# Kernel optimization log

Hardware: AMD Instinct MI355X
Metric: run time of the kernel (lower is better)

Reference implementation:

```python
import jax, jax.numpy as jnp
import numpy as np

B, C, H, W = 128, 1, 256, 256
IN_DIM = 256      # = W
HID = 1024
OUT_DIM = 10


def _linear_init(key, fan_in, shape):
    bound = 1.0 / np.sqrt(fan_in)
    return jax.random.uniform(key, shape, jnp.float32, -bound, bound)


def _make_layer_params(key, in_dim, hid):
    # 4 gates in fixed order: forget, input, cell, output
    ks = jax.random.split(key, 4)
    Wi = _linear_init(ks[0], in_dim, (in_dim, 4 * hid))
    Wh = _linear_init(ks[1], hid, (hid, 4 * hid))
    bi = _linear_init(ks[2], in_dim, (4 * hid,))
    bh = _linear_init(ks[3], hid, (4 * hid,))
    return Wi, Wh, bi, bh


def setup_inputs() -> dict:
    key = jax.random.key(0)
    kx, k1, k2, kc, kh1, kc1, kh2, kc2 = jax.random.split(key, 8)
    Wi1, Wh1, bi1, bh1 = _make_layer_params(k1, IN_DIM, HID)
    Wi2, Wh2, bi2, bh2 = _make_layer_params(k2, HID, HID)
    kcw, kcb = jax.random.split(kc)
    Wc = _linear_init(kcw, HID, (HID, OUT_DIM))
    bc = _linear_init(kcb, HID, (OUT_DIM,))
    return {
        "x": jax.random.normal(kx, (B, C, H, W), jnp.float32),
        "h01": jax.random.normal(kh1, (B, HID), jnp.float32),
        "c01": jax.random.normal(kc1, (B, HID), jnp.float32),
        "h02": jax.random.normal(kh2, (B, HID), jnp.float32),
        "c02": jax.random.normal(kc2, (B, HID), jnp.float32),
        "Wi1": Wi1, "Wh1": Wh1, "bi1": bi1, "bh1": bh1,
        "Wi2": Wi2, "Wh2": Wh2, "bi2": bi2, "bh2": bh2,
        "Wc": Wc, "bc": bc,
    }


def _lstm_layer(x, Wi, Wh, bi, bh, h0, c0):
    """x: [B,T,D] -> hidden outputs [B,T,H]. Gate order: f, i, g(cell), o."""
    hid = Wh.shape[0]
    # Batched input projection for all timesteps at once: [B,T,4H]
    xproj = jnp.einsum('btd,dg->btg', x, Wi) + bi

    def step(carry, xp_t):
        h, c = carry
        z = xp_t + h @ Wh + bh                       # [B,4H]
        f, i, g, o = jnp.split(z, 4, axis=-1)
        f = jax.nn.sigmoid(f)
        i = jax.nn.sigmoid(i)
        g = jnp.tanh(g)
        o = jax.nn.sigmoid(o)
        c_new = c * f + i * g
        h_new = jnp.tanh(c_new) * o
        return (h_new, c_new), h_new

    _, hs = jax.lax.scan(step, (h0, c0), jnp.swapaxes(xproj, 0, 1))  # hs: [T,B,H]
    return jnp.swapaxes(hs, 0, 1)


def reference(x, h01, c01, h02, c02,
              Wi1, Wh1, bi1, bh1,
              Wi2, Wh2, bi2, bh2,
              Wc, bc):
    b = x.shape[0]
    seq = x.shape[1] * x.shape[2]                    # C*H
    xs = x.reshape(b, seq, IN_DIM)                   # [B,T,D]
    out1 = _lstm_layer(xs, Wi1, Wh1, bi1, bh1, h01, c01)
    out2 = _lstm_layer(out1, Wi2, Wh2, bi2, bh2, h02, c02)
    y = out2[:, -1, :] @ Wc + bc                     # [B, OUT_DIM]
    return y
```

## Files before the change

kernel.cpp:

```cpp
#include <hip/hip_runtime.h>

typedef _Float16 f16;
typedef __attribute__((ext_vector_type(8))) _Float16 f16x8;
typedef __attribute__((ext_vector_type(4))) _Float16 f16x4;
typedef __attribute__((ext_vector_type(16))) float f32x16;

#define B_ 128
#define HID_ 1024
#define BH_ (B_ * HID_)

__global__ __launch_bounds__(256) void k_cast_x(const float* __restrict__ x,
                                                f16* __restrict__ xf) {
    size_t g = (size_t)blockIdx.x * blockDim.x + threadIdx.x;
    size_t e = g * 4;
    const int d = (int)(e & 255);
    const int t = (int)((e >> 8) & 255);
    const int b = (int)(e >> 16);
    float4 v = ((const float4*)x)[g];
    f16x4 o = {(f16)v.x, (f16)v.y, (f16)v.z, (f16)v.w};
    *(f16x4*)(xf + ((size_t)t * B_ + b) * 256 + d) = o;
}

__global__ __launch_bounds__(256) void k_pack(const float* __restrict__ src,
                                              f16* __restrict__ dst,
                                              int Ktot, int koff) {
    __shared__ float tile[64][65];
    const int tx = threadIdx.x & 63, ty = threadIdx.x >> 6;
    const int r0 = blockIdx.y * 64, c0 = blockIdx.x * 64;
    #pragma unroll
    for (int r = ty; r < 64; r += 4)
        tile[r][tx] = src[(size_t)(r0 + r) * 4096 + c0 + tx];
    __syncthreads();
    const int k = koff + r0 + tx;
    #pragma unroll
    for (int rr = ty; rr < 64; rr += 4) {
        const int col = c0 + rr;
        const int g = col >> 10, hg = col & 1023;
        const int wg = hg >> 3, pcl = (g << 3) | (hg & 7);
        size_t off = ((size_t)wg * 32 + pcl) * Ktot + (((k >> 3) ^ (pcl & 7)) << 3) + (k & 7);
        dst[off] = (f16)tile[tx][rr];
    }
}

__global__ __launch_bounds__(256) void k_prep(
    const float* __restrict__ bi1, const float* __restrict__ bh1,
    const float* __restrict__ bi2, const float* __restrict__ bh2,
    const float* __restrict__ h01, const float* __restrict__ h02,
    float* b1, float* b2, f16* h1r, f16* h2b, unsigned int* cnt) {
    int i = blockIdx.x * blockDim.x + threadIdx.x;
    if (i == 0) *cnt = 0u;
    if (i < 4096) { b1[i] = bi1[i] + bh1[i]; b2[i] = bi2[i] + bh2[i]; }
    if (i < BH_) {
        h1r[i] = (f16)h01[i];
        h2b[BH_ + i] = (f16)h02[i];
    }
}

__device__ __forceinline__ void publish8(f16* p, f16x4 v) {
    union { f16x4 h; unsigned long long u; } cv;
    cv.h = v;
    __hip_atomic_store((unsigned long long*)p, cv.u,
                       __ATOMIC_RELAXED, __HIP_MEMORY_SCOPE_AGENT);
}

__global__ __launch_bounds__(256, 1) void k_persist(
    const f16* __restrict__ Wp1,
    const f16* __restrict__ Wp2,
    const f16* __restrict__ xall,
    f16* h1r, f16* h2b,
    float* h2f,
    const float* __restrict__ b1, const float* __restrict__ b2,
    const float* __restrict__ c01, const float* __restrict__ c02,
    unsigned int* cnt) {
    __shared__ __align__(16) unsigned char smem[163840];
    f16*   Wl = (f16*)smem;
    float* zl = (float*)(smem + 131072);

    const int bid = blockIdx.x;
    const int layer = bid >> 7;
    const int wg = bid & 127;
    const int tid = threadIdx.x;
    const int lane = tid & 63, wave = tid >> 6, hl = lane >> 5;
    const int K = layer ? 2048 : 1280;

    {
        const f16* Wsrc = layer ? (Wp2 + (size_t)wg * 32 * 2048)
                                : (Wp1 + (size_t)wg * 32 * 1280);
        const int n = 32 * K / 8;
        for (int i = tid; i < n; i += 256)
            ((f16x8*)Wl)[i] = ((const f16x8*)Wsrc)[i];
    }

    const int m = tid & 127, half = tid >> 7;
    const int ug0 = wg * 8 + half * 4;
    const float* csrc = layer ? c02 : c01;
    float4 creg = *(const float4*)(csrc + (size_t)m * HID_ + ug0);
    float biasr[4][4];
    {
        const float* bsrc = layer ? b2 : b1;
        #pragma unroll
        for (int g = 0; g < 4; ++g)
            #pragma unroll
            for (int j = 0; j < 4; ++j)
                biasr[g][j] = bsrc[g * HID_ + ug0 + j];
    }
    __syncthreads();

    const int pcl = lane & 31;
    const int swz = pcl & 7;
    f16* hmine = (layer ? h2b : h1r);

    f32x16 acc[4];
    #pragma unroll
    for (int mt = 0; mt < 4; ++mt)
        #pragma unroll
        for (int r = 0; r < 16; ++r) acc[mt][r] = 0.f;

    if (layer == 0) {
        const f16* A0n = xall;
        for (int c = wave; c < 16; c += 4) {
            const int ic = c * 2 + hl;
            f16x8 bfrag = *(const f16x8*)(Wl + pcl * 1280 + ((ic ^ swz) << 3));
            const f16* ap = A0n + (size_t)pcl * 256 + c * 16 + hl * 8;
            #pragma unroll
            for (int mt = 0; mt < 4; ++mt) {
                f16x8 afrag = *(const f16x8*)(ap + (size_t)mt * 32 * 256);
                acc[mt] = __builtin_amdgcn_mfma_f32_32x32x16_f16(afrag, bfrag, acc[mt], 0, 0, 0);
            }
        }
    }

    for (int s = 0; s <= 256; ++s) {
        const bool active = layer == 0 ? (s < 256) : (s >= 1);
        if (active) {
            if (layer == 0) {
                const f16* A1 = h1r + (size_t)(s & 1) * BH_;
                for (int c = 16 + wave; c < 80; c += 4) {
                    const int ic = c * 2 + hl;
                    f16x8 bfrag = *(const f16x8*)(Wl + pcl * 1280 + ((ic ^ swz) << 3));
                    const f16* ap = A1 + (size_t)pcl * HID_ + (c * 16 - 256) + hl * 8;
                    #pragma unroll
                    for (int mt = 0; mt < 4; ++mt) {
                        f16x8 afrag = *(const f16x8*)(ap + (size_t)mt * 32 * HID_);
                        acc[mt] = __builtin_amdgcn_mfma_f32_32x32x16_f16(afrag, bfrag, acc[mt], 0, 0, 0);
                    }
                }
            } else {
                const f16* A0 = h1r + (size_t)(s & 1) * BH_;
                const f16* A1 = h2b + (size_t)(s & 1) * BH_;
                for (int c = wave; c < 128; c += 4) {
                    const f16* Ab = (c < 64) ? A0 : A1;
                    const int kloc = (c & 63) * 16;
                    const int ic = c * 2 + hl;
                    f16x8 bfrag = *(const f16x8*)(Wl + pcl * 2048 + ((ic ^ swz) << 3));
                    const f16* ap = Ab + (size_t)pcl * HID_ + kloc + hl * 8;
                    #pragma unroll
                    for (int mt = 0; mt < 4; ++mt) {
                        f16x8 afrag = *(const f16x8*)(ap + (size_t)mt * 32 * HID_);
                        acc[mt] = __builtin_amdgcn_mfma_f32_32x32x16_f16(afrag, bfrag, acc[mt], 0, 0, 0);
                    }
                }
            }

            float* Z = zl + (size_t)(wave & 1) * 4096;
            if (wave < 2) {
                #pragma unroll
                for (int mt = 0; mt < 4; ++mt)
                    #pragma unroll
                    for (int r = 0; r < 16; ++r) {
                        const int row = mt * 32 + (r & 3) + 8 * (r >> 2) + 4 * hl;
                        Z[row * 32 + (pcl ^ (row & 31))] = acc[mt][r];
                    }
            }
            __syncthreads();
            if (wave >= 2) {
                #pragma unroll
                for (int mt = 0; mt < 4; ++mt)
                    #pragma unroll
                    for (int r = 0; r < 16; ++r) {
                        const int row = mt * 32 + (r & 3) + 8 * (r >> 2) + 4 * hl;
                        Z[row * 32 + (pcl ^ (row & 31))] += acc[mt][r];
                    }
            }
            __syncthreads();

            float zg4[4][4];
            #pragma unroll
            for (int g = 0; g < 4; ++g)
                #pragma unroll
                for (int j = 0; j < 4; ++j) {
                    const int cc = g * 8 + half * 4 + j;
                    const int idx = m * 32 + (cc ^ (m & 31));
                    zg4[g][j] = zl[idx] + zl[4096 + idx] + biasr[g][j];
                }
            f16x4 hout;
            float4 hf;
            #pragma unroll
            for (int j = 0; j < 4; ++j) {
                const float fg = 1.f / (1.f + __expf(-zg4[0][j]));
                const float ig = 1.f / (1.f + __expf(-zg4[1][j]));
                const float gg = 1.f - 2.f / (__expf(2.f * zg4[2][j]) + 1.f);
                const float og = 1.f / (1.f + __expf(-zg4[3][j]));
                float cv = j == 0 ? creg.x : j == 1 ? creg.y : j == 2 ? creg.z : creg.w;
                const float cn = cv * fg + ig * gg;
                if (j == 0) creg.x = cn; else if (j == 1) creg.y = cn;
                else if (j == 2) creg.z = cn; else creg.w = cn;
                const float h = (1.f - 2.f / (__expf(2.f * cn) + 1.f)) * og;
                hout[j] = (f16)h;
                ((float*)&hf)[j] = h;
            }
            publish8(hmine + (size_t)((s + 1) & 1) * BH_ + (size_t)m * HID_ + ug0, hout);
            if (layer == 1 && s == 256)
                *(float4*)(h2f + (size_t)m * HID_ + ug0) = hf;
        }

        if (s < 256) {
            asm volatile("s_waitcnt vmcnt(0)" ::: "memory");
            __syncthreads();
            if (tid == 0)
                __hip_atomic_fetch_add(cnt, 1u, __ATOMIC_RELAXED, __HIP_MEMORY_SCOPE_AGENT);

            #pragma unroll
            for (int mt = 0; mt < 4; ++mt)
                #pragma unroll
                for (int r = 0; r < 16; ++r) acc[mt][r] = 0.f;
            if (layer == 0 && s + 1 < 256) {
                const f16* A0n = xall + (size_t)(s + 1) * (B_ * 256);
                for (int c = wave; c < 16; c += 4) {
                    const int ic = c * 2 + hl;
                    f16x8 bfrag = *(const f16x8*)(Wl + pcl * 1280 + ((ic ^ swz) << 3));
                    const f16* ap = A0n + (size_t)pcl * 256 + c * 16 + hl * 8;
                    #pragma unroll
                    for (int mt = 0; mt < 4; ++mt) {
                        f16x8 afrag = *(const f16x8*)(ap + (size_t)mt * 32 * 256);
                        acc[mt] = __builtin_amdgcn_mfma_f32_32x32x16_f16(afrag, bfrag, acc[mt], 0, 0, 0);
                    }
                }
            }

            if (tid == 0) {
                const unsigned int target = 256u * (unsigned)(s + 1);
                while (__hip_atomic_load(cnt, __ATOMIC_RELAXED, __HIP_MEMORY_SCOPE_AGENT) < target)
                    __builtin_amdgcn_s_sleep(8);
                __builtin_amdgcn_fence(__ATOMIC_ACQUIRE, "agent");
            }
            __syncthreads();
        }
    }
}

__global__ __launch_bounds__(64) void k_final(const float* __restrict__ h2f,
                                              const float* __restrict__ Wc,
                                              const float* __restrict__ bc,
                                              float* __restrict__ y) {
    const int b = blockIdx.x, lane = threadIdx.x;
    float acc[10] = {0, 0, 0, 0, 0, 0, 0, 0, 0, 0};
    for (int k = lane; k < HID_; k += 64) {
        const float h = h2f[b * HID_ + k];
        #pragma unroll
        for (int j = 0; j < 10; ++j) acc[j] = fmaf(h, Wc[k * 10 + j], acc[j]);
    }
    #pragma unroll
    for (int off = 32; off; off >>= 1)
        #pragma unroll
        for (int j = 0; j < 10; ++j) acc[j] += __shfl_down(acc[j], off);
    if (lane == 0) {
        #pragma unroll
        for (int j = 0; j < 10; ++j) y[b * 10 + j] = acc[j] + bc[j];
    }
}

extern "C" void kernel_launch(void* const* d_in, const int* in_sizes, int n_in,
                              void* d_out, int out_size, void* d_ws, size_t ws_size,
                              hipStream_t stream) {
    (void)in_sizes; (void)n_in; (void)out_size; (void)ws_size;
    const float* x   = (const float*)d_in[0];
    const float* h01 = (const float*)d_in[1];
    const float* c01 = (const float*)d_in[2];
    const float* h02 = (const float*)d_in[3];
    const float* c02 = (const float*)d_in[4];
    const float* Wi1 = (const float*)d_in[5];
    const float* Wh1 = (const float*)d_in[6];
    const float* bi1 = (const float*)d_in[7];
    const float* bh1 = (const float*)d_in[8];
    const float* Wi2 = (const float*)d_in[9];
    const float* Wh2 = (const float*)d_in[10];
    const float* bi2 = (const float*)d_in[11];
    const float* bh2 = (const float*)d_in[12];
    const float* Wc  = (const float*)d_in[13];
    const float* bc  = (const float*)d_in[14];
    float* y = (float*)d_out;

    char* w = (char*)d_ws;
    f16*   xall = (f16*)(w + 0);
    f16*   Wp1  = (f16*)(w + 16777216);
    f16*   Wp2  = (f16*)(w + 27262976);
    f16*   h1r  = (f16*)(w + 44040192);
    f16*   h2b  = (f16*)(w + 44564480);
    float* h2f  = (float*)(w + 45088768);
    float* b1   = (float*)(w + 45613056);
    float* b2   = (float*)(w + 45629440);
    unsigned int* cnt = (unsigned int*)(w + 45645824);

    k_cast_x<<<8192, 256, 0, stream>>>(x, xall);
    k_pack<<<dim3(64, 4),  256, 0, stream>>>(Wi1, Wp1, 1280, 0);
    k_pack<<<dim3(64, 16), 256, 0, stream>>>(Wh1, Wp1, 1280, 256);
    k_pack<<<dim3(64, 16), 256, 0, stream>>>(Wi2, Wp2, 2048, 0);
    k_pack<<<dim3(64, 16), 256, 0, stream>>>(Wh2, Wp2, 2048, 1024);
    k_prep<<<512, 256, 0, stream>>>(bi1, bh1, bi2, bh2, h01, h02, b1, b2, h1r, h2b, cnt);

    k_persist<<<256, 256, 0, stream>>>(Wp1, Wp2, xall, h1r, h2b, h2f, b1, b2, c01, c02, cnt);

    k_final<<<128, 64, 0, stream>>>(h2f, Wc, bc, y);
}
```

Before: 7.917 ms.

## Replace global step barrier with per-block flag dataflow sync and 512-thread blocks

Replaces the single global atomic counter barrier with per-workgroup progress flags per layer, polled by one wave across all 128 flags. Layer 0 can now run up to three steps ahead of layer 1 using a 4-slot h1 ring, and layer 1 starts its h1 half of the GEMM before waiting on its own layer's h2. Blocks grow from 256 to 512 threads (8 waves split the K loop), and the partial-sum reduction uses LDS atomics. This is meant to remove lockstep barrier stalls and skew between layers, at the cost of more polling traffic and LDS atomic contention.

```diff
diff --git a/kernel.cpp b/kernel.cpp
--- a/kernel.cpp
+++ b/kernel.cpp
@@ -46,32 +46,42 @@
     const float* __restrict__ bi1, const float* __restrict__ bh1,
     const float* __restrict__ bi2, const float* __restrict__ bh2,
     const float* __restrict__ h01, const float* __restrict__ h02,
-    float* b1, float* b2, f16* h1r, f16* h2b, unsigned int* cnt) {
+    float* b1, float* b2, f16* h1r, f16* h2b,
+    unsigned* flags1, unsigned* flags2) {
     int i = blockIdx.x * blockDim.x + threadIdx.x;
-    if (i == 0) *cnt = 0u;
+    if (i < 128) { flags1[i] = 0u; flags2[i] = 0u; }
     if (i < 4096) { b1[i] = bi1[i] + bh1[i]; b2[i] = bi2[i] + bh2[i]; }
     if (i < BH_) {
         h1r[i] = (f16)h01[i];
-        h2b[BH_ + i] = (f16)h02[i];
-    }
-}
-
-__device__ __forceinline__ void publish8(f16* p, f16x4 v) {
-    union { f16x4 h; unsigned long long u; } cv;
-    cv.h = v;
-    __hip_atomic_store((unsigned long long*)p, cv.u,
+        h2b[i] = (f16)h02[i];
+    }
+}
+
+__device__ __forceinline__ void publish4(f16* p, f16 a, f16 b) {
+    union { struct { f16 x, y; } h; unsigned u; } cv;
+    cv.h.x = a; cv.h.y = b;
+    __hip_atomic_store((unsigned*)p, cv.u,
                        __ATOMIC_RELAXED, __HIP_MEMORY_SCOPE_AGENT);
 }
 
-__global__ __launch_bounds__(256, 1) void k_persist(
-    const f16* __restrict__ Wp1,
-    const f16* __restrict__ Wp2,
+__device__ __forceinline__ void poll_ge(const unsigned* flags, int target) {
+    if (target <= 0) return;
+    const int l2 = (threadIdx.x & 63) << 1;
+    for (;;) {
+        int f0 = (int)__hip_atomic_load(flags + l2,     __ATOMIC_RELAXED, __HIP_MEMORY_SCOPE_AGENT);
+        int f1 = (int)__hip_atomic_load(flags + l2 + 1, __ATOMIC_RELAXED, __HIP_MEMORY_SCOPE_AGENT);
+        if (__all(f0 >= target && f1 >= target)) break;
+        __builtin_amdgcn_s_sleep(2);
+    }
+}
+
+__global__ __launch_bounds__(512, 1) void k_persist(
+    const f16* __restrict__ Wp1, const f16* __restrict__ Wp2,
     const f16* __restrict__ xall,
-    f16* h1r, f16* h2b,
-    float* h2f,
+    f16* h1r, f16* h2b, float* h2f,
     const float* __restrict__ b1, const float* __restrict__ b2,
     const float* __restrict__ c01, const float* __restrict__ c02,
-    unsigned int* cnt) {
+    unsigned* flags1, unsigned* flags2) {
     __shared__ __align__(16) unsigned char smem[163840];
     f16*   Wl = (f16*)smem;
     float* zl = (float*)(smem + 131072);
@@ -81,34 +91,34 @@
     const int wg = bid & 127;
     const int tid = threadIdx.x;
     const int lane = tid & 63, wave = tid >> 6, hl = lane >> 5;
+    const int pcl = lane & 31, swz = pcl & 7;
     const int K = layer ? 2048 : 1280;
 
     {
         const f16* Wsrc = layer ? (Wp2 + (size_t)wg * 32 * 2048)
                                 : (Wp1 + (size_t)wg * 32 * 1280);
         const int n = 32 * K / 8;
-        for (int i = tid; i < n; i += 256)
+        for (int i = tid; i < n; i += 512)
             ((f16x8*)Wl)[i] = ((const f16x8*)Wsrc)[i];
     }
 
-    const int m = tid & 127, half = tid >> 7;
-    const int ug0 = wg * 8 + half * 4;
+    const int m = tid & 127, q = tid >> 7;
+    const int u0 = q * 2;
+    const int ug0 = wg * 8 + u0;
     const float* csrc = layer ? c02 : c01;
-    float4 creg = *(const float4*)(csrc + (size_t)m * HID_ + ug0);
-    float biasr[4][4];
+    float c0 = csrc[(size_t)m * HID_ + ug0];
+    float c1v = csrc[(size_t)m * HID_ + ug0 + 1];
+    float biasr[4][2];
     {
         const float* bsrc = layer ? b2 : b1;
         #pragma unroll
-        for (int g = 0; g < 4; ++g)
-            #pragma unroll
-            for (int j = 0; j < 4; ++j)
-                biasr[g][j] = bsrc[g * HID_ + ug0 + j];
-    }
-    __syncthreads();
-
-    const int pcl = lane & 31;
-    const int swz = pcl & 7;
-    f16* hmine = (layer ? h2b : h1r);
+        for (int g = 0; g < 4; ++g) {
+            biasr[g][0] = bsrc[g * HID_ + ug0];
+            biasr[g][1] = bsrc[g * HID_ + ug0 + 1];
+        }
+    }
+    unsigned* myflags = layer ? flags2 : flags1;
+    f16* hmine = layer ? h2b : h1r;
 
     f32x16 acc[4];
     #pragma unroll
@@ -116,136 +126,136 @@
         #pragma unroll
         for (int r = 0; r < 16; ++r) acc[mt][r] = 0.f;
 
-    if (layer == 0) {
-        const f16* A0n = xall;
-        for (int c = wave; c < 16; c += 4) {
-            const int ic = c * 2 + hl;
-            f16x8 bfrag = *(const f16x8*)(Wl + pcl * 1280 + ((ic ^ swz) << 3));
-            const f16* ap = A0n + (size_t)pcl * 256 + c * 16 + hl * 8;
-            #pragma unroll
-            for (int mt = 0; mt < 4; ++mt) {
-                f16x8 afrag = *(const f16x8*)(ap + (size_t)mt * 32 * 256);
-                acc[mt] = __builtin_amdgcn_mfma_f32_32x32x16_f16(afrag, bfrag, acc[mt], 0, 0, 0);
-            }
-        }
-    }
-
-    for (int s = 0; s <= 256; ++s) {
-        const bool active = layer == 0 ? (s < 256) : (s >= 1);
-        if (active) {
-            if (layer == 0) {
-                const f16* A1 = h1r + (size_t)(s & 1) * BH_;
-                for (int c = 16 + wave; c < 80; c += 4) {
-                    const int ic = c * 2 + hl;
-                    f16x8 bfrag = *(const f16x8*)(Wl + pcl * 1280 + ((ic ^ swz) << 3));
-                    const f16* ap = A1 + (size_t)pcl * HID_ + (c * 16 - 256) + hl * 8;
-                    #pragma unroll
-                    for (int mt = 0; mt < 4; ++mt) {
-                        f16x8 afrag = *(const f16x8*)(ap + (size_t)mt * 32 * HID_);
-                        acc[mt] = __builtin_amdgcn_mfma_f32_32x32x16_f16(afrag, bfrag, acc[mt], 0, 0, 0);
-                    }
-                }
-            } else {
-                const f16* A0 = h1r + (size_t)(s & 1) * BH_;
-                const f16* A1 = h2b + (size_t)(s & 1) * BH_;
-                for (int c = wave; c < 128; c += 4) {
-                    const f16* Ab = (c < 64) ? A0 : A1;
-                    const int kloc = (c & 63) * 16;
-                    const int ic = c * 2 + hl;
-                    f16x8 bfrag = *(const f16x8*)(Wl + pcl * 2048 + ((ic ^ swz) << 3));
-                    const f16* ap = Ab + (size_t)pcl * HID_ + kloc + hl * 8;
-                    #pragma unroll
-                    for (int mt = 0; mt < 4; ++mt) {
-                        f16x8 afrag = *(const f16x8*)(ap + (size_t)mt * 32 * HID_);
-                        acc[mt] = __builtin_amdgcn_mfma_f32_32x32x16_f16(afrag, bfrag, acc[mt], 0, 0, 0);
-                    }
-                }
-            }
-
-            float* Z = zl + (size_t)(wave & 1) * 4096;
-            if (wave < 2) {
-                #pragma unroll
-                for (int mt = 0; mt < 4; ++mt)
-                    #pragma unroll
-                    for (int r = 0; r < 16; ++r) {
-                        const int row = mt * 32 + (r & 3) + 8 * (r >> 2) + 4 * hl;
-                        Z[row * 32 + (pcl ^ (row & 31))] = acc[mt][r];
-                    }
+    __syncthreads();
+
+    for (int t = 0; t < 256; ++t) {
+        if (layer == 0) {
+            const f16* A0 = xall + (size_t)t * (B_ * 256);
+            for (int c = wave; c < 16; c += 8) {
+                const int ic = c * 2 + hl;
+                f16x8 bfrag = *(const f16x8*)(Wl + pcl * 1280 + ((ic ^ swz) << 3));
+                const f16* ap = A0 + (size_t)pcl * 256 + c * 16 + hl * 8;
+                #pragma unroll
+                for (int mt = 0; mt < 4; ++mt) {
+                    f16x8 afrag = *(const f16x8*)(ap + (size_t)mt * 32 * 256);
+                    acc[mt] = __builtin_amdgcn_mfma_f32_32x32x16_f16(afrag, bfrag, acc[mt], 0, 0, 0);
+                }
+            }
+            if (wave == 0) {
+                poll_ge(flags1, t);
+                __builtin_amdgcn_fence(__ATOMIC_ACQUIRE, "agent");
+            } else if (wave == 1) {
+                poll_ge(flags2, t - 3);
             }
             __syncthreads();
-            if (wave >= 2) {
-                #pragma unroll
-                for (int mt = 0; mt < 4; ++mt)
-                    #pragma unroll
-                    for (int r = 0; r < 16; ++r) {
-                        const int row = mt * 32 + (r & 3) + 8 * (r >> 2) + 4 * hl;
-                        Z[row * 32 + (pcl ^ (row & 31))] += acc[mt][r];
-                    }
+            const f16* A1 = h1r + (size_t)(t & 3) * BH_;
+            for (int c = 16 + wave; c < 80; c += 8) {
+                const int ic = c * 2 + hl;
+                f16x8 bfrag = *(const f16x8*)(Wl + pcl * 1280 + ((ic ^ swz) << 3));
+                const f16* ap = A1 + (size_t)pcl * HID_ + (c * 16 - 256) + hl * 8;
+                #pragma unroll
+                for (int mt = 0; mt < 4; ++mt) {
+                    f16x8 afrag = *(const f16x8*)(ap + (size_t)mt * 32 * HID_);
+                    acc[mt] = __builtin_amdgcn_mfma_f32_32x32x16_f16(afrag, bfrag, acc[mt], 0, 0, 0);
+                }
+            }
+        } else {
+            if (wave == 0) {
+                poll_ge(flags1, t + 1);
+                __builtin_amdgcn_fence(__ATOMIC_ACQUIRE, "agent");
             }
             __syncthreads();
-
-            float zg4[4][4];
-            #pragma unroll
-            for (int g = 0; g < 4; ++g)
-                #pragma unroll
-                for (int j = 0; j < 4; ++j) {
-                    const int cc = g * 8 + half * 4 + j;
-                    const int idx = m * 32 + (cc ^ (m & 31));
-                    zg4[g][j] = zl[idx] + zl[4096 + idx] + biasr[g][j];
-                }
-            f16x4 hout;
-            float4 hf;
-            #pragma unroll
-            for (int j = 0; j < 4; ++j) {
-                const float fg = 1.f / (1.f + __expf(-zg4[0][j]));
-                const float ig = 1.f / (1.f + __expf(-zg4[1][j]));
-                const float gg = 1.f - 2.f / (__expf(2.f * zg4[2][j]) + 1.f);
-                const float og = 1.f / (1.f + __expf(-zg4[3][j]));
-                float cv = j == 0 ? creg.x : j == 1 ? creg.y : j == 2 ? creg.z : creg.w;
-                const float cn = cv * fg + ig * gg;
-                if (j == 0) creg.x = cn; else if (j == 1) creg.y = cn;
-                else if (j == 2) creg.z = cn; else creg.w = cn;
-                const float h = (1.f - 2.f / (__expf(2.f * cn) + 1.f)) * og;
-                hout[j] = (f16)h;
-                ((float*)&hf)[j] = h;
-            }
-            publish8(hmine + (size_t)((s + 1) & 1) * BH_ + (size_t)m * HID_ + ug0, hout);
-            if (layer == 1 && s == 256)
-                *(float4*)(h2f + (size_t)m * HID_ + ug0) = hf;
-        }
-
-        if (s < 256) {
-            asm volatile("s_waitcnt vmcnt(0)" ::: "memory");
+            const f16* A0 = h1r + (size_t)((t + 1) & 3) * BH_;
+            for (int c = wave; c < 64; c += 8) {
+                const int ic = c * 2 + hl;
+                f16x8 bfrag = *(const f16x8*)(Wl + pcl * 2048 + ((ic ^ swz) << 3));
+                const f16* ap = A0 + (size_t)pcl * HID_ + c * 16 + hl * 8;
+                #pragma unroll
+                for (int mt = 0; mt < 4; ++mt) {
+                    f16x8 afrag = *(const f16x8*)(ap + (size_t)mt * 32 * HID_);
+                    acc[mt] = __builtin_amdgcn_mfma_f32_32x32x16_f16(afrag, bfrag, acc[mt], 0, 0, 0);
+                }
+            }
+            if (wave == 0) {
+                poll_ge(flags2, t);
+                __builtin_amdgcn_fence(__ATOMIC_ACQUIRE, "agent");
+            }
             __syncthreads();
-            if (tid == 0)
-                __hip_atomic_fetch_add(cnt, 1u, __ATOMIC_RELAXED, __HIP_MEMORY_SCOPE_AGENT);
-
+            const f16* A1 = h2b + (size_t)(t & 1) * BH_;
+            for (int c = 64 + wave; c < 128; c += 8) {
+                const int ic = c * 2 + hl;
+                f16x8 bfrag = *(const f16x8*)(Wl + pcl * 2048 + ((ic ^ swz) << 3));
+                const f16* ap = A1 + (size_t)pcl * HID_ + (c * 16 - 1024) + hl * 8;
+                #pragma unroll
+                for (int mt = 0; mt < 4; ++mt) {
+                    f16x8 afrag = *(const f16x8*)(ap + (size_t)mt * 32 * HID_);
+                    acc[mt] = __builtin_amdgcn_mfma_f32_32x32x16_f16(afrag, bfrag, acc[mt], 0, 0, 0);
+                }
+            }
+        }
+
+        float* Z = zl + (size_t)(wave & 1) * 4096;
+        if (wave < 2) {
             #pragma unroll
             for (int mt = 0; mt < 4; ++mt)
                 #pragma unroll
-                for (int r = 0; r < 16; ++r) acc[mt][r] = 0.f;
-            if (layer == 0 && s + 1 < 256) {
-                const f16* A0n = xall + (size_t)(s + 1) * (B_ * 256);
-                for (int c = wave; c < 16; c += 4) {
-                    const int ic = c * 2 + hl;
-                    f16x8 bfrag = *(const f16x8*)(Wl + pcl * 1280 + ((ic ^ swz) << 3));
-                    const f16* ap = A0n + (size_t)pcl * 256 + c * 16 + hl * 8;
-                    #pragma unroll
-                    for (int mt = 0; mt < 4; ++mt) {
-                        f16x8 afrag = *(const f16x8*)(ap + (size_t)mt * 32 * 256);
-                        acc[mt] = __builtin_amdgcn_mfma_f32_32x32x16_f16(afrag, bfrag, acc[mt], 0, 0, 0);
-                    }
-                }
-            }
-
-            if (tid == 0) {
-                const unsigned int target = 256u * (unsigned)(s + 1);
-                while (__hip_atomic_load(cnt, __ATOMIC_RELAXED, __HIP_MEMORY_SCOPE_AGENT) < target)
-                    __builtin_amdgcn_s_sleep(8);
-                __builtin_amdgcn_fence(__ATOMIC_ACQUIRE, "agent");
-            }
-            __syncthreads();
-        }
+                for (int r = 0; r < 16; ++r) {
+                    const int row = mt * 32 + (r & 3) + 8 * (r >> 2) + 4 * hl;
+                    Z[row * 32 + (pcl ^ (row & 31))] = acc[mt][r];
+                }
+        }
+        __syncthreads();
+        if (wave >= 2) {
+            #pragma unroll
+            for (int mt = 0; mt < 4; ++mt)
+                #pragma unroll
+                for (int r = 0; r < 16; ++r) {
+                    const int row = mt * 32 + (r & 3) + 8 * (r >> 2) + 4 * hl;
+                    atomicAdd(&Z[row * 32 + (pcl ^ (row & 31))], acc[mt][r]);
+                }
+        }
+        __syncthreads();
+        #pragma unroll
+        for (int mt = 0; mt < 4; ++mt)
+            #pragma unroll
+            for (int r = 0; r < 16; ++r) acc[mt][r] = 0.f;
+
+        float zg[4][2];
+        #pragma unroll
+        for (int g = 0; g < 4; ++g)
+            #pragma unroll
+            for (int j = 0; j < 2; ++j) {
+                const int cc = g * 8 + u0 + j;
+                const int idx = m * 32 + (cc ^ (m & 31));
+                zg[g][j] = zl[idx] + zl[4096 + idx] + biasr[g][j];
+            }
+        f16 ho[2];
+        float hf[2];
+        #pragma unroll
+        for (int j = 0; j < 2; ++j) {
+            const float fg = 1.f / (1.f + __expf(-zg[0][j]));
+            const float ig = 1.f / (1.f + __expf(-zg[1][j]));
+            const float gg = 1.f - 2.f / (__expf(2.f * zg[2][j]) + 1.f);
+            const float og = 1.f / (1.f + __expf(-zg[3][j]));
+            const float cv = j ? c1v : c0;
+            const float cn = cv * fg + ig * gg;
+            if (j) c1v = cn; else c0 = cn;
+            const float h = (1.f - 2.f / (__expf(2.f * cn) + 1.f)) * og;
+            ho[j] = (f16)h;
+            hf[j] = h;
+        }
+        const int wslot = layer ? ((t + 1) & 1) : ((t + 1) & 3);
+        publish4(hmine + (size_t)wslot * BH_ + (size_t)m * HID_ + ug0, ho[0], ho[1]);
+        if (layer == 1 && t == 255) {
+            h2f[(size_t)m * HID_ + ug0]     = hf[0];
+            h2f[(size_t)m * HID_ + ug0 + 1] = hf[1];
+        }
+
+        asm volatile("s_waitcnt vmcnt(0)" ::: "memory");
+        __syncthreads();
+        if (tid == 0)
+            __hip_atomic_store(myflags + wg, (unsigned)(t + 1),
+                               __ATOMIC_RELAXED, __HIP_MEMORY_SCOPE_AGENT);
     }
 }
 
@@ -296,20 +306,23 @@
     f16*   Wp1  = (f16*)(w + 16777216);
     f16*   Wp2  = (f16*)(w + 27262976);
     f16*   h1r  = (f16*)(w + 44040192);
-    f16*   h2b  = (f16*)(w + 44564480);
-    float* h2f  = (float*)(w + 45088768);
-    float* b1   = (float*)(w + 45613056);
-    float* b2   = (float*)(w + 45629440);
-    unsigned int* cnt = (unsigned int*)(w + 45645824);
+    f16*   h2b  = (f16*)(w + 45088768);
+    float* h2f  = (float*)(w + 45613056);
+    float* b1   = (float*)(w + 46137344);
+    float* b2   = (float*)(w + 46153728);
+    unsigned* flags1 = (unsigned*)(w + 46170112);
+    unsigned* flags2 = (unsigned*)(w + 46170624);
 
     k_cast_x<<<8192, 256, 0, stream>>>(x, xall);
     k_pack<<<dim3(64, 4),  256, 0, stream>>>(Wi1, Wp1, 1280, 0);
     k_pack<<<dim3(64, 16), 256, 0, stream>>>(Wh1, Wp1, 1280, 256);
     k_pack<<<dim3(64, 16), 256, 0, stream>>>(Wi2, Wp2, 2048, 0);
     k_pack<<<dim3(64, 16), 256, 0, stream>>>(Wh2, Wp2, 2048, 1024);
-    k_prep<<<512, 256, 0, stream>>>(bi1, bh1, bi2, bh2, h01, h02, b1, b2, h1r, h2b, cnt);
-
-    k_persist<<<256, 256, 0, stream>>>(Wp1, Wp2, xall, h1r, h2b, h2f, b1, b2, c01, c02, cnt);
+    k_prep<<<512, 256, 0, stream>>>(bi1, bh1, bi2, bh2, h01, h02,
+                                    b1, b2, h1r, h2b, flags1, flags2);
+
+    k_persist<<<256, 512, 0, stream>>>(Wp1, Wp2, xall, h1r, h2b, h2f,
+                                       b1, b2, c01, c02, flags1, flags2);
 
     k_final<<<128, 64, 0, stream>>>(h2f, Wc, bc, y);
 }
```

New measurement: 12.85 ms. 62.3% more time.
